# Performance work log

Measured on AMD Instinct MI355X. Metric: run time of the kernel, lower is better.

The kernel has to match this reference:

```python
import jax, jax.numpy as jnp
import numpy as np

N_NODES = 50000
N_EDGES = 600000
D_IN = 128
H = D_IN // 2  # 64
N_GRAPHS = 500
DIM_TARGET = 1


def setup_inputs() -> dict:
    key = jax.random.key(0)
    ks = jax.random.split(key, 16)
    x = jax.random.normal(ks[0], (N_NODES, D_IN), dtype=jnp.float32)
    edge_index = jax.random.randint(ks[1], (2, N_EDGES), 0, N_NODES, dtype=jnp.int64)
    batch = jnp.sort(jax.random.randint(ks[2], (N_NODES,), 0, N_GRAPHS, dtype=jnp.int64))
    # SAGEConv params: lin_l (neighbor aggregate, with bias), lin_r (root, no bias)
    s = 1.0 / np.sqrt(D_IN)
    Wl = jax.random.uniform(ks[3], (D_IN, H), jnp.float32, -s, s)
    bl = jnp.zeros((H,), jnp.float32)
    Wr = jax.random.uniform(ks[4], (D_IN, H), jnp.float32, -s, s)
    # MLP: 64->32->16->8->1
    dims = [H, H // 2, H // 4, H // 8, DIM_TARGET]
    params = {}
    for i in range(4):
        si = 1.0 / np.sqrt(dims[i])
        params[f"W{i}"] = jax.random.uniform(ks[5 + 2 * i], (dims[i], dims[i + 1]), jnp.float32, -si, si)
        params[f"b{i}"] = jax.random.uniform(ks[6 + 2 * i], (dims[i + 1],), jnp.float32, -si, si)
    return dict(x=x, edge_index=edge_index, batch=batch, Wl=Wl, bl=bl, Wr=Wr, **params)


def reference(x, edge_index, batch, Wl, bl, Wr, W0, b0, W1, b1, W2, b2, W3, b3):
    n_nodes = x.shape[0]
    src, dst = edge_index[0], edge_index[1]
    # SAGEConv mean aggregation: mean of source-node features at each target node
    agg = jax.ops.segment_sum(x[src], dst, num_segments=n_nodes)          # [N, D]
    cnt = jax.ops.segment_sum(jnp.ones((src.shape[0],), x.dtype), dst, num_segments=n_nodes)
    mean_nbr = agg / jnp.maximum(cnt, 1.0)[:, None]
    x1 = mean_nbr @ Wl + bl + x @ Wr                                      # [N, H]
    # global_mean_pool by graph id
    gsum = jax.ops.segment_sum(x1, batch, num_segments=N_GRAPHS)          # [G, H]
    gcnt = jax.ops.segment_sum(jnp.ones((n_nodes,), x.dtype), batch, num_segments=N_GRAPHS)
    h = gsum / jnp.maximum(gcnt, 1.0)[:, None]
    # MLP (dropout is identity in eval mode)
    h = jax.nn.relu(h @ W0 + b0)
    h = jax.nn.relu(h @ W1 + b1)
    h = jax.nn.relu(h @ W2 + b2)
    return h @ W3 + b3
```

## Files before the change

kernel.cpp:

```cpp
#include <hip/hip_runtime.h>
#include <hip/hip_bf16.h>

#define N_NODES  50000
#define N_EDGES  600000
#define D_IN     128
#define H        64
#define N_GRAPHS 500
#define MAXDEG   48

#define CONV_BLOCKS 6250
#define SCAT_CHUNKS 512
#define SCAT_BLOCKS (SCAT_CHUNKS * 8)
#define EPC         1172
#define NPS         (N_NODES / 8)
#define GST_BLOCKS  2

#define SPLIT    16
#define GBLK     (N_GRAPHS * SPLIT)

#define OF_DEG   0
#define MEMSET_B 200704
#define OF_PNP   200704
#define OF_PX    4296704
#define OF_GCNT  4552704
#define OF_GST   4554752
#define OF_COL   4558848
#define OF_XB    9358848

__device__ __forceinline__ float bflo(unsigned int u) { return __uint_as_float(u << 16); }
__device__ __forceinline__ float bfhi(unsigned int u) { return __uint_as_float(u & 0xffff0000u); }

__global__ __launch_bounds__(256) void prep_kernel(
        const float* __restrict__ x, unsigned short* __restrict__ xb,
        const int* __restrict__ src, const int* __restrict__ dst,
        int* __restrict__ deg, unsigned short* __restrict__ col,
        const int* __restrict__ batch, int* __restrict__ gstart) {
    int bid = blockIdx.x, t = threadIdx.x;
    if (bid < CONV_BLOCKS) {
        int i = bid * 256 + t;
        float4 f = ((const float4*)x)[i];
        ushort4 u;
        u.x = __bfloat16_as_ushort(__float2bfloat16(f.x));
        u.y = __bfloat16_as_ushort(__float2bfloat16(f.y));
        u.z = __bfloat16_as_ushort(__float2bfloat16(f.z));
        u.w = __bfloat16_as_ushort(__float2bfloat16(f.w));
        ((ushort4*)xb)[i] = u;
    } else if (bid < CONV_BLOCKS + SCAT_BLOCKS) {
        int rel   = bid - CONV_BLOCKS;
        int shard = bid & 7;
        int chunk = rel >> 3;
        int lo = shard * NPS, hi = lo + NPS;
        int e0 = chunk * EPC;
        int e1 = e0 + EPC; if (e1 > N_EDGES) e1 = N_EDGES;
        for (int e = e0 + t; e < e1; e += 256) {
            int d = dst[e];
            if (d >= lo && d < hi) {
                int pos = atomicAdd(&deg[d], 1);
                if (pos < MAXDEG)
                    col[(size_t)d * MAXDEG + pos] = (unsigned short)src[e];
            }
        }
    } else {
        int g = (bid - CONV_BLOCKS - SCAT_BLOCKS) * 256 + t;
        if (g <= N_GRAPHS) {
            int lo = 0, hi = N_NODES;
            while (lo < hi) {
                int m = (lo + hi) >> 1;
                if (batch[m] < g) lo = m + 1; else hi = m;
            }
            gstart[g] = lo;
        }
    }
}

__global__ __launch_bounds__(256) void gather_kernel(
        const unsigned short* __restrict__ xb, const unsigned short* __restrict__ col,
        const int* __restrict__ deg, const int* __restrict__ gstart,
        float* __restrict__ PnP, float* __restrict__ Px, int* __restrict__ gcnt) {
    __shared__ float red[4 * D_IN];
    int bid  = blockIdx.x;
    int wave = threadIdx.x >> 6;
    int lane = threadIdx.x & 63;

    if (bid < GBLK) {
        int g = bid >> 4;
        int s = bid & 15;
        int n0 = gstart[g], n1 = gstart[g + 1];
        const unsigned short* xl = xb + 2 * lane;

        float2 pn = make_float2(0.f, 0.f);
        for (int n = n0 + s * 4 + wave; n < n1; n += 4 * SPLIT) {
            int d = deg[n];
            int dl = (d < MAXDEG) ? d : MAXDEG;
            const unsigned short* cl = col + (size_t)n * MAXDEG;
            int cidx = (lane < dl) ? (int)cl[lane] : 0;

            float2 t = make_float2(0.f, 0.f);
            int j = 0;
            for (; j + 8 <= dl; j += 8) {
                int s0 = __shfl(cidx, j),     s1 = __shfl(cidx, j + 1);
                int s2 = __shfl(cidx, j + 2), s3 = __shfl(cidx, j + 3);
                int s4 = __shfl(cidx, j + 4), s5 = __shfl(cidx, j + 5);
                int s6 = __shfl(cidx, j + 6), s7 = __shfl(cidx, j + 7);
                unsigned int u0 = *(const unsigned int*)(xl + (size_t)s0 * D_IN);
                unsigned int u1 = *(const unsigned int*)(xl + (size_t)s1 * D_IN);
                unsigned int u2 = *(const unsigned int*)(xl + (size_t)s2 * D_IN);
                unsigned int u3 = *(const unsigned int*)(xl + (size_t)s3 * D_IN);
                unsigned int u4 = *(const unsigned int*)(xl + (size_t)s4 * D_IN);
                unsigned int u5 = *(const unsigned int*)(xl + (size_t)s5 * D_IN);
                unsigned int u6 = *(const unsigned int*)(xl + (size_t)s6 * D_IN);
                unsigned int u7 = *(const unsigned int*)(xl + (size_t)s7 * D_IN);
                t.x += bflo(u0) + bflo(u1) + bflo(u2) + bflo(u3)
                     + bflo(u4) + bflo(u5) + bflo(u6) + bflo(u7);
                t.y += bfhi(u0) + bfhi(u1) + bfhi(u2) + bfhi(u3)
                     + bfhi(u4) + bfhi(u5) + bfhi(u6) + bfhi(u7);
            }
            for (; j + 4 <= dl; j += 4) {
                int s0 = __shfl(cidx, j),     s1 = __shfl(cidx, j + 1);
                int s2 = __shfl(cidx, j + 2), s3 = __shfl(cidx, j + 3);
                unsigned int u0 = *(const unsigned int*)(xl + (size_t)s0 * D_IN);
                unsigned int u1 = *(const unsigned int*)(xl + (size_t)s1 * D_IN);
                unsigned int u2 = *(const unsigned int*)(xl + (size_t)s2 * D_IN);
                unsigned int u3 = *(const unsigned int*)(xl + (size_t)s3 * D_IN);
                t.x += bflo(u0) + bflo(u1) + bflo(u2) + bflo(u3);
                t.y += bfhi(u0) + bfhi(u1) + bfhi(u2) + bfhi(u3);
            }
            for (; j < dl; ++j) {
                int sn = __shfl(cidx, j);
                unsigned int u = *(const unsigned int*)(xl + (size_t)sn * D_IN);
                t.x += bflo(u); t.y += bfhi(u);
            }
            if (d > 0) {
                float w = __builtin_amdgcn_rcpf((float)d);
                pn.x = fmaf(t.x, w, pn.x);
                pn.y = fmaf(t.y, w, pn.y);
            }
        }
        red[wave * D_IN + 2 * lane]     = pn.x;
        red[wave * D_IN + 2 * lane + 1] = pn.y;
        __syncthreads();
        if (threadIdx.x < D_IN) {
            float v = red[threadIdx.x] + red[D_IN + threadIdx.x]
                    + red[2 * D_IN + threadIdx.x] + red[3 * D_IN + threadIdx.x];
            PnP[(size_t)bid * D_IN + threadIdx.x] = v;
        }
    } else {
        int p  = bid - GBLK;
        int n0 = gstart[p], n1 = gstart[p + 1];
        float fx = 0.f, fy = 0.f;
        for (int n = n0 + wave; n < n1; n += 4) {
            unsigned int u = *(const unsigned int*)(xb + (size_t)n * D_IN + 2 * lane);
            fx += bflo(u); fy += bfhi(u);
        }
        red[wave * D_IN + 2 * lane]     = fx;
        red[wave * D_IN + 2 * lane + 1] = fy;
        __syncthreads();
        if (threadIdx.x < D_IN) {
            float v = red[threadIdx.x] + red[D_IN + threadIdx.x]
                    + red[2 * D_IN + threadIdx.x] + red[3 * D_IN + threadIdx.x];
            Px[(size_t)p * D_IN + threadIdx.x] = v;
        }
        if (threadIdx.x == 0) gcnt[p] = n1 - n0;
    }
}

__global__ void final_kernel(
        const float* __restrict__ PnP, const float* __restrict__ Px,
        const int* __restrict__ gcnt,
        const float* __restrict__ Wl, const float* __restrict__ bl,
        const float* __restrict__ Wr,
        const float* __restrict__ W0, const float* __restrict__ b0,
        const float* __restrict__ W1, const float* __restrict__ b1,
        const float* __restrict__ W2, const float* __restrict__ b2,
        const float* __restrict__ W3, const float* __restrict__ b3,
        float* __restrict__ out) {
    int g = blockIdx.x;
    int t = threadIdx.x;
    __shared__ float sp[D_IN], sx[D_IN], hs[H], a0[32], a1[16], a2[8];
    {
        const float* base = PnP + ((size_t)g << 4) * D_IN + t;
        float v = 0.f;
        #pragma unroll
        for (int s = 0; s < SPLIT; ++s) v += base[s * D_IN];
        sp[t] = v;
        sx[t] = Px[(size_t)g * D_IN + t];
    }
    __syncthreads();

    int ng = gcnt[g];
    if (t < H) {
        float acc = 0.f;
        #pragma unroll 8
        for (int d = 0; d < D_IN; ++d)
            acc += sp[d] * Wl[d * H + t] + sx[d] * Wr[d * H + t];
        hs[t] = (ng > 0) ? (acc / (float)ng + bl[t]) : 0.f;
    }
    __syncthreads();
    if (t < 32) { float a = b0[t]; for (int d = 0; d < H;  ++d) a += hs[d] * W0[d * 32 + t]; a0[t] = fmaxf(a, 0.f); }
    __syncthreads();
    if (t < 16) { float a = b1[t]; for (int d = 0; d < 32; ++d) a += a0[d] * W1[d * 16 + t]; a1[t] = fmaxf(a, 0.f); }
    __syncthreads();
    if (t < 8)  { float a = b2[t]; for (int d = 0; d < 16; ++d) a += a1[d] * W2[d * 8 + t];  a2[t] = fmaxf(a, 0.f); }
    __syncthreads();
    if (t == 0) { float a = b3[0]; for (int d = 0; d < 8;  ++d) a += a2[d] * W3[d]; out[g] = a; }
}

extern "C" void kernel_launch(void* const* d_in, const int* in_sizes, int n_in,
                              void* d_out, int out_size, void* d_ws, size_t ws_size,
                              hipStream_t stream) {
    const float* x     = (const float*)d_in[0];
    const int*   ei    = (const int*)  d_in[1];
    const int*   batch = (const int*)  d_in[2];
    const float* Wl    = (const float*)d_in[3];
    const float* bl    = (const float*)d_in[4];
    const float* Wr    = (const float*)d_in[5];
    const float* W0    = (const float*)d_in[6];
    const float* b0    = (const float*)d_in[7];
    const float* W1    = (const float*)d_in[8];
    const float* b1    = (const float*)d_in[9];
    const float* W2    = (const float*)d_in[10];
    const float* b2    = (const float*)d_in[11];
    const float* W3    = (const float*)d_in[12];
    const float* b3    = (const float*)d_in[13];
    float* out = (float*)d_out;

    char* ws = (char*)d_ws;
    int*            deg    = (int*)(ws + OF_DEG);
    float*          PnP    = (float*)(ws + OF_PNP);
    float*          Px     = (float*)(ws + OF_PX);
    int*            gcnt   = (int*)(ws + OF_GCNT);
    int*            gstart = (int*)(ws + OF_GST);
    unsigned short* col    = (unsigned short*)(ws + OF_COL);
    unsigned short* xb     = (unsigned short*)(ws + OF_XB);

    hipMemsetAsync(ws, 0, MEMSET_B, stream);

    prep_kernel<<<CONV_BLOCKS + SCAT_BLOCKS + GST_BLOCKS, 256, 0, stream>>>(
        x, xb, ei, ei + N_EDGES, deg, col, batch, gstart);
    gather_kernel<<<GBLK + N_GRAPHS, 256, 0, stream>>>(
        xb, col, deg, gstart, PnP, Px, gcnt);
    final_kernel<<<N_GRAPHS, 128, 0, stream>>>(PnP, Px, gcnt, Wl, bl, Wr,
                                               W0, b0, W1, b1, W2, b2, W3, b3, out);
}
```

Before: 168.0 us.

## Project x by Wl with MFMA before gathering to halve gather width

Because mean aggregation is linear, the prep kernel now computes y = x·Wl in bf16 with MFMA instructions, and the neighbour gather reads 64-wide rows of y instead of 128-wide rows of x. The per-graph sum of x for the root term moves into the prep kernel and reads fp32 x directly. Each wave now covers two neighbours at once, with each half-wave reading a 32-bit slice of a row. This is meant to cut random gather traffic and PnP size in half. In exchange the prep kernel carries a small GEMM, Wl is rounded to bf16, and the Wr loop in the final kernel stays per-graph.

```diff
diff --git a/kernel.cpp b/kernel.cpp
--- a/kernel.cpp
+++ b/kernel.cpp
@@ -8,12 +8,15 @@
 #define N_GRAPHS 500
 #define MAXDEG   48
 
-#define CONV_BLOCKS 6250
+#define PROJ_BLOCKS 782
+#define M_TILES     3125
 #define SCAT_CHUNKS 512
 #define SCAT_BLOCKS (SCAT_CHUNKS * 8)
 #define EPC         1172
 #define NPS         (N_NODES / 8)
 #define GST_BLOCKS  2
+#define PX_BLOCKS   500
+#define PREP_GRID   (PROJ_BLOCKS + SCAT_BLOCKS + GST_BLOCKS + PX_BLOCKS)
 
 #define SPLIT    16
 #define GBLK     (N_GRAPHS * SPLIT)
@@ -21,34 +24,73 @@
 #define OF_DEG   0
 #define MEMSET_B 200704
 #define OF_PNP   200704
-#define OF_PX    4296704
-#define OF_GCNT  4552704
-#define OF_GST   4554752
-#define OF_COL   4558848
-#define OF_XB    9358848
+#define OF_PX    2248704
+#define OF_GCNT  2504704
+#define OF_GST   2506752
+#define OF_COL   2508800
+#define OF_YB    7308800
+
+typedef __attribute__((ext_vector_type(8))) short short8;
+typedef __attribute__((ext_vector_type(4))) float float4v;
 
 __device__ __forceinline__ float bflo(unsigned int u) { return __uint_as_float(u << 16); }
 __device__ __forceinline__ float bfhi(unsigned int u) { return __uint_as_float(u & 0xffff0000u); }
+__device__ __forceinline__ unsigned short f2bf(float f) {
+    return __bfloat16_as_ushort(__float2bfloat16(f));
+}
 
 __global__ __launch_bounds__(256) void prep_kernel(
-        const float* __restrict__ x, unsigned short* __restrict__ xb,
+        const float* __restrict__ x, const float* __restrict__ Wl,
+        unsigned short* __restrict__ yb,
         const int* __restrict__ src, const int* __restrict__ dst,
         int* __restrict__ deg, unsigned short* __restrict__ col,
-        const int* __restrict__ batch, int* __restrict__ gstart) {
+        const int* __restrict__ batch, int* __restrict__ gstart,
+        float* __restrict__ Px, int* __restrict__ gcnt) {
+    __shared__ float red[512];
     int bid = blockIdx.x, t = threadIdx.x;
-    if (bid < CONV_BLOCKS) {
-        int i = bid * 256 + t;
-        float4 f = ((const float4*)x)[i];
-        ushort4 u;
-        u.x = __bfloat16_as_ushort(__float2bfloat16(f.x));
-        u.y = __bfloat16_as_ushort(__float2bfloat16(f.y));
-        u.z = __bfloat16_as_ushort(__float2bfloat16(f.z));
-        u.w = __bfloat16_as_ushort(__float2bfloat16(f.w));
-        ((ushort4*)xb)[i] = u;
-    } else if (bid < CONV_BLOCKS + SCAT_BLOCKS) {
-        int rel   = bid - CONV_BLOCKS;
+    int wave = t >> 6, lane = t & 63;
+
+    if (bid < PROJ_BLOCKS) {
+        int mt = bid * 4 + wave;
+        if (mt < M_TILES) {
+            int c = lane & 15, q = lane >> 4;
+            short8 Bf[4][4];
+            #pragma unroll
+            for (int t4 = 0; t4 < 4; ++t4)
+                #pragma unroll
+                for (int s4 = 0; s4 < 4; ++s4) {
+                    short8 b;
+                    #pragma unroll
+                    for (int jj = 0; jj < 8; ++jj)
+                        b[jj] = (short)f2bf(Wl[(s4 * 32 + q * 8 + jj) * H + t4 * 16 + c]);
+                    Bf[t4][s4] = b;
+                }
+            float4v acc[4] = {};
+            const float* xrow = x + ((size_t)mt * 16 + c) * D_IN + q * 8;
+            #pragma unroll
+            for (int s4 = 0; s4 < 4; ++s4) {
+                const float4* ap = (const float4*)(xrow + s4 * 32);
+                float4 a0 = ap[0], a1 = ap[1];
+                short8 Af;
+                Af[0] = (short)f2bf(a0.x); Af[1] = (short)f2bf(a0.y);
+                Af[2] = (short)f2bf(a0.z); Af[3] = (short)f2bf(a0.w);
+                Af[4] = (short)f2bf(a1.x); Af[5] = (short)f2bf(a1.y);
+                Af[6] = (short)f2bf(a1.z); Af[7] = (short)f2bf(a1.w);
+                #pragma unroll
+                for (int t4 = 0; t4 < 4; ++t4)
+                    acc[t4] = __builtin_amdgcn_mfma_f32_16x16x32_bf16(Af, Bf[t4][s4], acc[t4], 0, 0, 0);
+            }
+            #pragma unroll
+            for (int t4 = 0; t4 < 4; ++t4)
+                #pragma unroll
+                for (int r = 0; r < 4; ++r) {
+                    int node = mt * 16 + q * 4 + r;
+                    yb[(size_t)node * H + t4 * 16 + c] = f2bf(acc[t4][r]);
+                }
+        }
+    } else if (bid < PROJ_BLOCKS + SCAT_BLOCKS) {
         int shard = bid & 7;
-        int chunk = rel >> 3;
+        int chunk = (bid - PROJ_BLOCKS) >> 3;
         int lo = shard * NPS, hi = lo + NPS;
         int e0 = chunk * EPC;
         int e1 = e0 + EPC; if (e1 > N_EDGES) e1 = N_EDGES;
@@ -60,8 +102,8 @@
                     col[(size_t)d * MAXDEG + pos] = (unsigned short)src[e];
             }
         }
-    } else {
-        int g = (bid - CONV_BLOCKS - SCAT_BLOCKS) * 256 + t;
+    } else if (bid < PROJ_BLOCKS + SCAT_BLOCKS + GST_BLOCKS) {
+        int g = (bid - PROJ_BLOCKS - SCAT_BLOCKS) * 256 + t;
         if (g <= N_GRAPHS) {
             int lo = 0, hi = N_NODES;
             while (lo < hi) {
@@ -70,105 +112,97 @@
             }
             gstart[g] = lo;
         }
+    } else {
+        int p = bid - PROJ_BLOCKS - SCAT_BLOCKS - GST_BLOCKS;
+        int lo = 0, hi = N_NODES;
+        while (lo < hi) { int m = (lo + hi) >> 1; if (batch[m] < p) lo = m + 1; else hi = m; }
+        int a = lo;
+        hi = N_NODES;
+        while (lo < hi) { int m = (lo + hi) >> 1; if (batch[m] < p + 1) lo = m + 1; else hi = m; }
+        int b = lo;
+        float fx = 0.f, fy = 0.f;
+        for (int n = a + wave; n < b; n += 4) {
+            float2 u = ((const float2*)(x + (size_t)n * D_IN))[lane];
+            fx += u.x; fy += u.y;
+        }
+        red[wave * D_IN + 2 * lane]     = fx;
+        red[wave * D_IN + 2 * lane + 1] = fy;
+        __syncthreads();
+        if (t < D_IN) {
+            float v = red[t] + red[D_IN + t] + red[2 * D_IN + t] + red[3 * D_IN + t];
+            Px[(size_t)p * D_IN + t] = v;
+        }
+        if (t == 0) gcnt[p] = b - a;
     }
 }
 
 __global__ __launch_bounds__(256) void gather_kernel(
-        const unsigned short* __restrict__ xb, const unsigned short* __restrict__ col,
+        const unsigned short* __restrict__ yb, const unsigned short* __restrict__ col,
         const int* __restrict__ deg, const int* __restrict__ gstart,
-        float* __restrict__ PnP, float* __restrict__ Px, int* __restrict__ gcnt) {
-    __shared__ float red[4 * D_IN];
+        float* __restrict__ PnP) {
+    __shared__ float red[4 * H];
     int bid  = blockIdx.x;
     int wave = threadIdx.x >> 6;
     int lane = threadIdx.x & 63;
-
-    if (bid < GBLK) {
-        int g = bid >> 4;
-        int s = bid & 15;
-        int n0 = gstart[g], n1 = gstart[g + 1];
-        const unsigned short* xl = xb + 2 * lane;
-
-        float2 pn = make_float2(0.f, 0.f);
-        for (int n = n0 + s * 4 + wave; n < n1; n += 4 * SPLIT) {
-            int d = deg[n];
-            int dl = (d < MAXDEG) ? d : MAXDEG;
-            const unsigned short* cl = col + (size_t)n * MAXDEG;
-            int cidx = (lane < dl) ? (int)cl[lane] : 0;
-
-            float2 t = make_float2(0.f, 0.f);
-            int j = 0;
-            for (; j + 8 <= dl; j += 8) {
-                int s0 = __shfl(cidx, j),     s1 = __shfl(cidx, j + 1);
-                int s2 = __shfl(cidx, j + 2), s3 = __shfl(cidx, j + 3);
-                int s4 = __shfl(cidx, j + 4), s5 = __shfl(cidx, j + 5);
-                int s6 = __shfl(cidx, j + 6), s7 = __shfl(cidx, j + 7);
-                unsigned int u0 = *(const unsigned int*)(xl + (size_t)s0 * D_IN);
-                unsigned int u1 = *(const unsigned int*)(xl + (size_t)s1 * D_IN);
-                unsigned int u2 = *(const unsigned int*)(xl + (size_t)s2 * D_IN);
-                unsigned int u3 = *(const unsigned int*)(xl + (size_t)s3 * D_IN);
-                unsigned int u4 = *(const unsigned int*)(xl + (size_t)s4 * D_IN);
-                unsigned int u5 = *(const unsigned int*)(xl + (size_t)s5 * D_IN);
-                unsigned int u6 = *(const unsigned int*)(xl + (size_t)s6 * D_IN);
-                unsigned int u7 = *(const unsigned int*)(xl + (size_t)s7 * D_IN);
-                t.x += bflo(u0) + bflo(u1) + bflo(u2) + bflo(u3)
-                     + bflo(u4) + bflo(u5) + bflo(u6) + bflo(u7);
-                t.y += bfhi(u0) + bfhi(u1) + bfhi(u2) + bfhi(u3)
-                     + bfhi(u4) + bfhi(u5) + bfhi(u6) + bfhi(u7);
-            }
-            for (; j + 4 <= dl; j += 4) {
-                int s0 = __shfl(cidx, j),     s1 = __shfl(cidx, j + 1);
-                int s2 = __shfl(cidx, j + 2), s3 = __shfl(cidx, j + 3);
-                unsigned int u0 = *(const unsigned int*)(xl + (size_t)s0 * D_IN);
-                unsigned int u1 = *(const unsigned int*)(xl + (size_t)s1 * D_IN);
-                unsigned int u2 = *(const unsigned int*)(xl + (size_t)s2 * D_IN);
-                unsigned int u3 = *(const unsigned int*)(xl + (size_t)s3 * D_IN);
-                t.x += bflo(u0) + bflo(u1) + bflo(u2) + bflo(u3);
-                t.y += bfhi(u0) + bfhi(u1) + bfhi(u2) + bfhi(u3);
-            }
-            for (; j < dl; ++j) {
-                int sn = __shfl(cidx, j);
-                unsigned int u = *(const unsigned int*)(xl + (size_t)sn * D_IN);
-                t.x += bflo(u); t.y += bfhi(u);
-            }
-            if (d > 0) {
-                float w = __builtin_amdgcn_rcpf((float)d);
-                pn.x = fmaf(t.x, w, pn.x);
-                pn.y = fmaf(t.y, w, pn.y);
-            }
-        }
-        red[wave * D_IN + 2 * lane]     = pn.x;
-        red[wave * D_IN + 2 * lane + 1] = pn.y;
-        __syncthreads();
-        if (threadIdx.x < D_IN) {
-            float v = red[threadIdx.x] + red[D_IN + threadIdx.x]
-                    + red[2 * D_IN + threadIdx.x] + red[3 * D_IN + threadIdx.x];
-            PnP[(size_t)bid * D_IN + threadIdx.x] = v;
-        }
-    } else {
-        int p  = bid - GBLK;
-        int n0 = gstart[p], n1 = gstart[p + 1];
-        float fx = 0.f, fy = 0.f;
-        for (int n = n0 + wave; n < n1; n += 4) {
-            unsigned int u = *(const unsigned int*)(xb + (size_t)n * D_IN + 2 * lane);
-            fx += bflo(u); fy += bfhi(u);
-        }
-        red[wave * D_IN + 2 * lane]     = fx;
-        red[wave * D_IN + 2 * lane + 1] = fy;
-        __syncthreads();
-        if (threadIdx.x < D_IN) {
-            float v = red[threadIdx.x] + red[D_IN + threadIdx.x]
-                    + red[2 * D_IN + threadIdx.x] + red[3 * D_IN + threadIdx.x];
-            Px[(size_t)p * D_IN + threadIdx.x] = v;
-        }
-        if (threadIdx.x == 0) gcnt[p] = n1 - n0;
+    int half = lane >> 5, fp = lane & 31;
+    int g = bid >> 4, s = bid & 15;
+    int n0 = gstart[g], n1 = gstart[g + 1];
+    const unsigned short* yl = yb + 2 * fp;
+
+    float2 pn = make_float2(0.f, 0.f);
+    for (int n = n0 + s * 4 + wave; n < n1; n += 4 * SPLIT) {
+        int d = deg[n];
+        int dl = (d < MAXDEG) ? d : MAXDEG;
+        int cidx = (lane < dl) ? (int)col[(size_t)n * MAXDEG + lane] : 0;
+
+        float tx = 0.f, ty = 0.f;
+        int j = 0;
+        for (; j + 8 <= dl; j += 8) {
+            int s0 = __shfl(cidx, j + half),     s1 = __shfl(cidx, j + 2 + half);
+            int s2 = __shfl(cidx, j + 4 + half), s3 = __shfl(cidx, j + 6 + half);
+            unsigned int u0 = *(const unsigned int*)(yl + (size_t)s0 * H);
+            unsigned int u1 = *(const unsigned int*)(yl + (size_t)s1 * H);
+            unsigned int u2 = *(const unsigned int*)(yl + (size_t)s2 * H);
+            unsigned int u3 = *(const unsigned int*)(yl + (size_t)s3 * H);
+            tx += bflo(u0) + bflo(u1) + bflo(u2) + bflo(u3);
+            ty += bfhi(u0) + bfhi(u1) + bfhi(u2) + bfhi(u3);
+        }
+        for (; j + 2 <= dl; j += 2) {
+            int s0 = __shfl(cidx, j + half);
+            unsigned int u = *(const unsigned int*)(yl + (size_t)s0 * H);
+            tx += bflo(u); ty += bfhi(u);
+        }
+        if (j < dl) {
+            int s0 = __shfl(cidx, j);
+            if (half == 0) {
+                unsigned int u = *(const unsigned int*)(yl + (size_t)s0 * H);
+                tx += bflo(u); ty += bfhi(u);
+            }
+        }
+        if (d > 0) {
+            float w = __builtin_amdgcn_rcpf((float)d);
+            pn.x = fmaf(tx, w, pn.x);
+            pn.y = fmaf(ty, w, pn.y);
+        }
+    }
+    pn.x += __shfl_xor(pn.x, 32);
+    pn.y += __shfl_xor(pn.y, 32);
+    if (half == 0) {
+        red[wave * H + 2 * fp]     = pn.x;
+        red[wave * H + 2 * fp + 1] = pn.y;
+    }
+    __syncthreads();
+    if (threadIdx.x < H) {
+        float v = red[threadIdx.x] + red[H + threadIdx.x]
+                + red[2 * H + threadIdx.x] + red[3 * H + threadIdx.x];
+        PnP[(size_t)bid * H + threadIdx.x] = v;
     }
 }
 
 __global__ void final_kernel(
         const float* __restrict__ PnP, const float* __restrict__ Px,
         const int* __restrict__ gcnt,
-        const float* __restrict__ Wl, const float* __restrict__ bl,
-        const float* __restrict__ Wr,
+        const float* __restrict__ bl, const float* __restrict__ Wr,
         const float* __restrict__ W0, const float* __restrict__ b0,
         const float* __restrict__ W1, const float* __restrict__ b1,
         const float* __restrict__ W2, const float* __restrict__ b2,
@@ -176,25 +210,23 @@
         float* __restrict__ out) {
     int g = blockIdx.x;
     int t = threadIdx.x;
-    __shared__ float sp[D_IN], sx[D_IN], hs[H], a0[32], a1[16], a2[8];
+    __shared__ float sx[D_IN], hs[H], a0[32], a1[16], a2[8];
+    sx[t]      = Px[(size_t)g * D_IN + t];
+    sx[t + 64] = Px[(size_t)g * D_IN + 64 + t];
+    float sp = 0.f;
     {
-        const float* base = PnP + ((size_t)g << 4) * D_IN + t;
-        float v = 0.f;
+        const float* base = PnP + ((size_t)g << 4) * H + t;
         #pragma unroll
-        for (int s = 0; s < SPLIT; ++s) v += base[s * D_IN];
-        sp[t] = v;
-        sx[t] = Px[(size_t)g * D_IN + t];
+        for (int s = 0; s < SPLIT; ++s) sp += base[s * H];
     }
     __syncthreads();
 
     int ng = gcnt[g];
-    if (t < H) {
-        float acc = 0.f;
-        #pragma unroll 8
-        for (int d = 0; d < D_IN; ++d)
-            acc += sp[d] * Wl[d * H + t] + sx[d] * Wr[d * H + t];
-        hs[t] = (ng > 0) ? (acc / (float)ng + bl[t]) : 0.f;
-    }
+    float acc = sp;
+    #pragma unroll 8
+    for (int d = 0; d < D_IN; ++d)
+        acc += sx[d] * Wr[d * H + t];
+    hs[t] = (ng > 0) ? (acc / (float)ng + bl[t]) : 0.f;
     __syncthreads();
     if (t < 32) { float a = b0[t]; for (int d = 0; d < H;  ++d) a += hs[d] * W0[d * 32 + t]; a0[t] = fmaxf(a, 0.f); }
     __syncthreads();
@@ -231,14 +263,13 @@
     int*            gcnt   = (int*)(ws + OF_GCNT);
     int*            gstart = (int*)(ws + OF_GST);
     unsigned short* col    = (unsigned short*)(ws + OF_COL);
-    unsigned short* xb     = (unsigned short*)(ws + OF_XB);
+    unsigned short* yb     = (unsigned short*)(ws + OF_YB);
 
     hipMemsetAsync(ws, 0, MEMSET_B, stream);
 
-    prep_kernel<<<CONV_BLOCKS + SCAT_BLOCKS + GST_BLOCKS, 256, 0, stream>>>(
-        x, xb, ei, ei + N_EDGES, deg, col, batch, gstart);
-    gather_kernel<<<GBLK + N_GRAPHS, 256, 0, stream>>>(
-        xb, col, deg, gstart, PnP, Px, gcnt);
-    final_kernel<<<N_GRAPHS, 128, 0, stream>>>(PnP, Px, gcnt, Wl, bl, Wr,
-                                               W0, b0, W1, b1, W2, b2, W3, b3, out);
-}
+    prep_kernel<<<PREP_GRID, 256, 0, stream>>>(
+        x, Wl, yb, ei, ei + N_EDGES, deg, col, batch, gstart, Px, gcnt);
+    gather_kernel<<<GBLK, 256, 0, stream>>>(yb, col, deg, gstart, PnP);
+    final_kernel<<<N_GRAPHS, 64, 0, stream>>>(PnP, Px, gcnt, bl, Wr,
+                                              W0, b0, W1, b1, W2, b2, W3, b3, out);
+}
```

Result: slower. 171.5 us (+2.1%).
